# Performance work log

Hardware: AMD Instinct MI355X
Metric: run time of the kernel (lower is better)

Reference implementation:

```python
import jax, jax.numpy as jnp
import numpy as np

STD = 1.0

def setup_inputs() -> dict:
    key = jax.random.key(0)
    k1, k2, k3 = jax.random.split(key, 3)
    B, G, D = 16384, 8192, 64
    return {
        "input": jax.random.normal(k1, (B, D), dtype=jnp.float32),
        "inputs": jax.random.normal(k2, (G, D), dtype=jnp.float32),
        "weights": jax.random.normal(k3, (G,), dtype=jnp.float32),
    }

def reference(input, inputs, weights):
    dot_prod = jnp.einsum("bd,gd->bg", input, inputs)
    norm_input = jnp.sum(input * input, axis=-1, keepdims=True)   # [B, 1]
    norm_inputs = jnp.sum(inputs * inputs, axis=-1)               # [G]
    distance = norm_input + norm_inputs - 2.0 * dot_prod          # [B, G]
    # Gaussian kernel weighted sum over centers -> [B]
    out = jnp.einsum("bg,g->b", jnp.exp(-distance / (2.0 * STD * STD)), weights)
    return out
```

## Files before the change

kernel.cpp:

```cpp
#include <hip/hip_runtime.h>


typedef __attribute__((ext_vector_type(8))) _Float16 half8v;
typedef __attribute__((ext_vector_type(16))) float f32x16;
typedef unsigned short u16;
typedef unsigned int u32;

#define L2E   1.4426950408889634f
#define NHL2E 0.72134752044448170f
#define GP 12

#define MFMA(a,b,c) __builtin_amdgcn_mfma_f32_32x32x16_f16(a,b,c,0,0,0)

__global__ __launch_bounds__(256)
void convert_C(const float* __restrict__ C, const float* __restrict__ W,
               _Float16* __restrict__ Cf, float2* __restrict__ cw, int G){
  int idx = blockIdx.x*256 + threadIdx.x;
  int g = idx >> 2, f = idx & 3;
  if (g >= G) return;
  const float* row = C + (size_t)g*64 + f*16;
  int cg = g >> 5, cl = g & 31;
  float norm = 0.f;
  _Float16 hv[16];
  #pragma unroll
  for (int q=0; q<4; q++){
    float4 v = *(const float4*)(row + q*4);
    float xv[4] = {v.x, v.y, v.z, v.w};
    #pragma unroll
    for (int e=0; e<4; e++){
      float x = xv[e];
      norm = fmaf(x, x, norm);
      hv[q*4+e] = (_Float16)x;
    }
  }
  norm += __shfl_xor(norm, 1);
  norm += __shfl_xor(norm, 2);
  size_t u = ((size_t)(cg*4 + f)*64 + cl)*8;
  *(half8v*)(Cf + u)       = *(half8v*)hv;
  *(half8v*)(Cf + u + 256) = *(half8v*)(hv + 8);
  if (f == 0) cw[g] = make_float2(-NHL2E*norm, W[g]);
}

__global__ __launch_bounds__(256, 3)
void rbf_mfma(const float* __restrict__ X, const _Float16* __restrict__ Cf,
              const float2* __restrict__ cw, float* __restrict__ out){
  const int tid = threadIdx.x;
  const int l  = tid & 63;
  const int cl = l & 31;
  const int h  = l >> 5;
  const int w  = tid >> 6;
  const int b  = blockIdx.x;
  const int gp = b % GP;
  const int rows0 = (b / GP) * 256 + w * 64;

  const int t0  = gp * 21 + (gp < 4 ? gp : 4);
  const int ntl = (gp < 4) ? 22 : 21;

  half8v af[2][4];
  float xn[2];
  #pragma unroll
  for (int rf=0; rf<2; rf++){
    const float* xr = X + (size_t)(rows0 + rf*32 + cl)*64;
    float s = 0.f;
    #pragma unroll
    for (int f=0; f<4; f++){
      float4 v0 = *(const float4*)(xr + f*16 + h*8);
      float4 v1 = *(const float4*)(xr + f*16 + h*8 + 4);
      float xv[8] = {v0.x,v0.y,v0.z,v0.w,v1.x,v1.y,v1.z,v1.w};
      _Float16 hv[8];
      #pragma unroll
      for (int e=0;e<8;e++){
        float x = xv[e];
        s = fmaf(x, x, s);
        hv[e] = (_Float16)x;
      }
      af[rf][f] = *(half8v*)hv;
    }
    s += __shfl_xor(s, 32);
    xn[rf] = -NHL2E * s;
  }

  const char* baseF = (const char*)Cf + (size_t)l*16;
  const float2* cwp = cw + cl;

  half8v bf[2];
  bf[0] = *(const half8v*)(baseF + (size_t)t0*4096);

  float racc0[16], racc1[16];
  #pragma unroll
  for (int r=0;r<16;r++){ racc0[r]=0.f; racc1[r]=0.f; }

  f32x16 aE0, aE1, aO0, aO1;
  float2 cwE, cwO;

  #define EPIX(P, R, CWV, RACC)                                             \
    RACC[R] = fmaf(__builtin_amdgcn_exp2f(fmaf(P[R], L2E, CWV.x)),          \
                   CWV.y, RACC[R])

  #define TILE(T, TN, C0, C1, P0, P1, CWC, CWP, DO_EPI) do {                \
    const int t_ = (T), tn_ = (TN);                                         \
    CWC = cwp[t_*32];                                                       \
    C0 = (f32x16){}; C1 = (f32x16){};                                       \
    _Pragma("unroll")                                                       \
    for (int f=0; f<4; ++f){                                                \
      const int p = f & 1, q = p ^ 1;                                       \
      const int nf = (f + 1) & 3;                                           \
      const int nt = (f == 3) ? tn_ : t_;                                   \
      bf[q] = *(const half8v*)(baseF + (size_t)nt*4096 + (size_t)nf*1024);  \
      C0 = MFMA(af[0][f], bf[p], C0);                                       \
      if (DO_EPI){                                                          \
        EPIX(P0, f*4+0, CWP, racc0); EPIX(P1, f*4+0, CWP, racc1);           \
        EPIX(P0, f*4+1, CWP, racc0); EPIX(P1, f*4+1, CWP, racc1);           \
      }                                                                     \
      C1 = MFMA(af[1][f], bf[p], C1);                                       \
      if (DO_EPI){                                                          \
        EPIX(P0, f*4+2, CWP, racc0); EPIX(P1, f*4+2, CWP, racc1);           \
        EPIX(P0, f*4+3, CWP, racc0); EPIX(P1, f*4+3, CWP, racc1);           \
      }                                                                     \
    }                                                                       \
  } while(0)

  TILE(t0, t0+1, aE0, aE1, aO0, aO1, cwE, cwO, 0);
  int ti = 1;
  #pragma unroll 1
  for (; ti + 1 < ntl; ti += 2){
    const int To = t0 + ti, Te = t0 + ti + 1;
    const int TnO = Te;
    const int TnE = (ti + 2 < ntl) ? Te + 1 : t0;
    TILE(To, TnO, aO0, aO1, aE0, aE1, cwO, cwE, 1);
    TILE(Te, TnE, aE0, aE1, aO0, aO1, cwE, cwO, 1);
  }
  if (ti < ntl){
    TILE(t0+ti, t0, aO0, aO1, aE0, aE1, cwO, cwE, 1);
    #pragma unroll
    for (int r=0;r<16;++r){ EPIX(aO0, r, cwO, racc0); EPIX(aO1, r, cwO, racc1); }
  } else {
    #pragma unroll
    for (int r=0;r<16;++r){ EPIX(aE0, r, cwE, racc0); EPIX(aE1, r, cwE, racc1); }
  }
  #undef TILE
  #undef EPIX

  #pragma unroll
  for (int rf=0; rf<2; rf++){
    #pragma unroll
    for (int r=0;r<16;r++){
      float v = rf ? racc1[r] : racc0[r];
      v += __shfl_xor(v, 1);
      v += __shfl_xor(v, 2);
      v += __shfl_xor(v, 4);
      v += __shfl_xor(v, 8);
      v += __shfl_xor(v, 16);
      const int rit = (r&3) + 8*(r>>2) + 4*h;
      const float xnv = __shfl(xn[rf], rit);
      if (cl == 0)
        atomicAdd(&out[rows0 + rf*32 + rit], v * __builtin_amdgcn_exp2f(xnv));
    }
  }
}

extern "C" void kernel_launch(void* const* d_in, const int* in_sizes, int n_in,
                              void* d_out, int out_size, void* d_ws, size_t ws_size,
                              hipStream_t stream) {
  const float* X = (const float*)d_in[0];
  const float* C = (const float*)d_in[1];
  const float* W = (const float*)d_in[2];
  float* out = (float*)d_out;
  const int B = in_sizes[0] / 64;
  const int G = in_sizes[2];

  _Float16* Cf = (_Float16*)d_ws;
  float2* cw = (float2*)(Cf + (size_t)G*64);

  hipMemsetAsync(out, 0, (size_t)B*sizeof(float), stream);
  convert_C<<<(G*4)/256, 256, 0, stream>>>(C, W, Cf, cw, G);
  rbf_mfma<<<(B/256)*GP, 256, 0, stream>>>(X, Cf, cw, out);
}
```

Baseline: 48.26 us.

## Skip Gaussian exponentials below a per-row threshold and drop software pipelining

Each output row gets a precomputed log2-domain threshold. A tile element's exp2 and weighted accumulate run only when some lane in the wavefront exceeds that threshold, so negligibly small kernel terms are skipped. The goal is to cut transcendental work, which dominates once the GEMM runs on MFMA. In exchange, the loop that interleaved the previous tile's epilogue with the current tile's MFMAs becomes a simple sequential loop, which loses that overlap and adds a compare and wave vote per element. Accuracy now rests on the cutoff being small relative to the output magnitude.

```diff
diff --git a/kernel.cpp b/kernel.cpp
--- a/kernel.cpp
+++ b/kernel.cpp
@@ -9,6 +9,7 @@
 #define L2E   1.4426950408889634f
 #define NHL2E 0.72134752044448170f
 #define GP 12
+#define SCREEN_THR -53.0f
 
 #define MFMA(a,b,c) __builtin_amdgcn_mfma_f32_32x32x16_f16(a,b,c,0,0,0)
 
@@ -80,6 +81,14 @@
     xn[rf] = -NHL2E * s;
   }
 
+  float thr0[16], thr1[16];
+  #pragma unroll
+  for (int r=0;r<16;++r){
+    const int rit = (r&3) + 8*(r>>2) + 4*h;
+    thr0[r] = SCREEN_THR - __shfl(xn[0], rit);
+    thr1[r] = SCREEN_THR - __shfl(xn[1], rit);
+  }
+
   const char* baseF = (const char*)Cf + (size_t)l*16;
   const float2* cwp = cw + cl;
 
@@ -90,56 +99,33 @@
   #pragma unroll
   for (int r=0;r<16;r++){ racc0[r]=0.f; racc1[r]=0.f; }
 
-  f32x16 aE0, aE1, aO0, aO1;
-  float2 cwE, cwO;
+  #pragma unroll 1
+  for (int ti = 0; ti < ntl; ++ti){
+    const int T  = t0 + ti;
+    const int TN = (ti+1 < ntl) ? T + 1 : t0;
+    const float2 cwv = cwp[T*32];
 
-  #define EPIX(P, R, CWV, RACC)                                             \
-    RACC[R] = fmaf(__builtin_amdgcn_exp2f(fmaf(P[R], L2E, CWV.x)),          \
-                   CWV.y, RACC[R])
+    f32x16 a0 = {}, a1 = {};
+    #pragma unroll
+    for (int f=0; f<4; ++f){
+      const int p = f & 1, q = p ^ 1;
+      const int nf = (f + 1) & 3;
+      const int nt_ = (f == 3) ? TN : T;
+      bf[q] = *(const half8v*)(baseF + (size_t)nt_*4096 + (size_t)nf*1024);
+      a0 = MFMA(af[0][f], bf[p], a0);
+      a1 = MFMA(af[1][f], bf[p], a1);
+    }
 
-  #define TILE(T, TN, C0, C1, P0, P1, CWC, CWP, DO_EPI) do {                \
-    const int t_ = (T), tn_ = (TN);                                         \
-    CWC = cwp[t_*32];                                                       \
-    C0 = (f32x16){}; C1 = (f32x16){};                                       \
-    _Pragma("unroll")                                                       \
-    for (int f=0; f<4; ++f){                                                \
-      const int p = f & 1, q = p ^ 1;                                       \
-      const int nf = (f + 1) & 3;                                           \
-      const int nt = (f == 3) ? tn_ : t_;                                   \
-      bf[q] = *(const half8v*)(baseF + (size_t)nt*4096 + (size_t)nf*1024);  \
-      C0 = MFMA(af[0][f], bf[p], C0);                                       \
-      if (DO_EPI){                                                          \
-        EPIX(P0, f*4+0, CWP, racc0); EPIX(P1, f*4+0, CWP, racc1);           \
-        EPIX(P0, f*4+1, CWP, racc0); EPIX(P1, f*4+1, CWP, racc1);           \
-      }                                                                     \
-      C1 = MFMA(af[1][f], bf[p], C1);                                       \
-      if (DO_EPI){                                                          \
-        EPIX(P0, f*4+2, CWP, racc0); EPIX(P1, f*4+2, CWP, racc1);           \
-        EPIX(P0, f*4+3, CWP, racc0); EPIX(P1, f*4+3, CWP, racc1);           \
-      }                                                                     \
-    }                                                                       \
-  } while(0)
-
-  TILE(t0, t0+1, aE0, aE1, aO0, aO1, cwE, cwO, 0);
-  int ti = 1;
-  #pragma unroll 1
-  for (; ti + 1 < ntl; ti += 2){
-    const int To = t0 + ti, Te = t0 + ti + 1;
-    const int TnO = Te;
-    const int TnE = (ti + 2 < ntl) ? Te + 1 : t0;
-    TILE(To, TnO, aO0, aO1, aE0, aE1, cwO, cwE, 1);
-    TILE(Te, TnE, aE0, aE1, aO0, aO1, cwE, cwO, 1);
+    #pragma unroll
+    for (int r=0;r<16;++r){
+      const float e0 = fmaf(a0[r], L2E, cwv.x);
+      if (__builtin_expect(__any(e0 > thr0[r]), 0))
+        racc0[r] = fmaf(__builtin_amdgcn_exp2f(e0), cwv.y, racc0[r]);
+      const float e1 = fmaf(a1[r], L2E, cwv.x);
+      if (__builtin_expect(__any(e1 > thr1[r]), 0))
+        racc1[r] = fmaf(__builtin_amdgcn_exp2f(e1), cwv.y, racc1[r]);
+    }
   }
-  if (ti < ntl){
-    TILE(t0+ti, t0, aO0, aO1, aE0, aE1, cwO, cwE, 1);
-    #pragma unroll
-    for (int r=0;r<16;++r){ EPIX(aO0, r, cwO, racc0); EPIX(aO1, r, cwO, racc1); }
-  } else {
-    #pragma unroll
-    for (int r=0;r<16;++r){ EPIX(aE0, r, cwE, racc0); EPIX(aE1, r, cwE, racc1); }
-  }
-  #undef TILE
-  #undef EPIX
 
   #pragma unroll
   for (int rf=0; rf<2; rf++){
```

Measured after the change: 58.34 us. +20.9%, slower.
